# Optimization experiments

Hardware: AMD Instinct MI355X
Metric: run time of the kernel (lower is better)

Reference implementation:

```python
import jax, jax.numpy as jnp
import numpy as np

B, T, D, H = 32, 512, 1024, 16
HD = D // H  # 64


def setup_inputs() -> dict:
    key = jax.random.key(0)
    ks = jax.random.split(key, 12)
    s_in = 1.0 / np.sqrt(D)
    x = jax.random.normal(ks[0], (B, T, D), dtype=jnp.float32)
    Wi = jax.random.normal(ks[1], (D, D), dtype=jnp.float32) * s_in
    bi = jnp.zeros((D,), dtype=jnp.float32)
    Wk = jax.random.normal(ks[2], (H, D, HD), dtype=jnp.float32) * s_in
    bk = jnp.zeros((H, HD), dtype=jnp.float32)
    Wq = jax.random.normal(ks[3], (H, D, HD), dtype=jnp.float32) * s_in
    bq = jnp.zeros((H, HD), dtype=jnp.float32)
    Wv = jax.random.normal(ks[4], (H, D, HD), dtype=jnp.float32) * s_in
    bv = jnp.zeros((H, HD), dtype=jnp.float32)
    Wo = jax.random.normal(ks[5], (D, D), dtype=jnp.float32) * s_in
    bo = jnp.zeros((D,), dtype=jnp.float32)
    return {"x": x, "Wi": Wi, "bi": bi, "Wk": Wk, "bk": bk,
            "Wq": Wq, "bq": bq, "Wv": Wv, "bv": bv, "Wo": Wo, "bo": bo}


def reference(x, Wi, bi, Wk, bk, Wq, bq, Wv, bv, Wo, bo):
    # in_proj
    h = x @ Wi + bi  # [B,T,D]
    # per-head K/Q/V projections, vectorized over heads
    k = jnp.einsum('btd,hde->bhte', h, Wk) + bk[None, :, None, :]  # [B,H,T,HD]
    q = jnp.einsum('btd,hde->bhte', h, Wq) + bq[None, :, None, :]
    v = jnp.einsum('btd,hde->bhte', h, Wv) + bv[None, :, None, :]
    # NOTE: original computes wei = k @ q^T (keys as rows), masks with tril,
    # softmax over last axis (queries). Faithfully reproduced (no scaling).
    wei = jnp.einsum('bhtd,bhsd->bhts', k, q)  # [B,H,T,T]
    causal = jnp.tril(jnp.ones((T, T), dtype=bool))
    wei = jnp.where(causal, wei, -jnp.inf)
    wei = jax.nn.softmax(wei, axis=-1)
    # dropout: eval mode (identity)
    out = jnp.einsum('bhts,bhsd->bhtd', wei, v)  # [B,H,T,HD]
    out = out.transpose(0, 2, 1, 3).reshape(B, T, D)  # concat heads on last dim
    return out @ Wo + bo
```

## Files before the change

### kernel.cpp

```cpp
#include <hip/hip_runtime.h>
#include <hip/hip_bf16.h>
#include <stdint.h>

#define NTOK 16384

typedef _Float16 f16;
typedef f16   f16x8 __attribute__((ext_vector_type(8)));
typedef float f32x4 __attribute__((ext_vector_type(4)));

__device__ __forceinline__ float bf2f(ushort h){
  union { uint32_t u; float f; } v; v.u = ((uint32_t)h) << 16; return v.f;
}
__device__ __forceinline__ ushort f2bf(float f){
  union { float f; uint32_t u; } v; v.f = f;
  uint32_t u = v.u;
  return (ushort)((u + 0x7FFFu + ((u >> 16) & 1u)) >> 16);
}
__device__ __forceinline__ ushort f2h(float f){
  return __builtin_bit_cast(ushort, (f16)f);
}
__device__ __forceinline__ f16x8 ld16(const ushort* p){
  uint4 u = *(const uint4*)p;
  return __builtin_bit_cast(f16x8, u);
}
__device__ __forceinline__ float ldf(const void* p, size_t idx, int isf32){
  if (isf32) return ((const float*)p)[idx];
  return bf2f(((const ushort*)p)[idx]);
}

__device__ __forceinline__ const ushort* swz(const ushort* base, uint row, uint chunk){
  return base + (size_t)row*64u + (size_t)((chunk ^ (row & 7u))*8u);
}

__device__ __forceinline__ void stage64(const ushort* g, uint strideEl,
                                        ushort* ldsbase, uint tid){
  uint w = tid >> 6;
  #pragma unroll
  for (int i = 0; i < 2; ++i){
    uint lc  = i*256u + tid;
    uint row = lc >> 3, cp = lc & 7u;
    uint c   = cp ^ (row & 7u);
    const ushort* gp = g + (size_t)row*strideEl + c*8u;
    ushort* lp = ldsbase + (size_t)(i*256u + w*64u)*8u;
    __builtin_amdgcn_global_load_lds((const __attribute__((address_space(1))) void*)gp,
        (__attribute__((address_space(3))) void*)lp, 16, 0, 0);
  }
}

__global__ __launch_bounds__(256) void kdetect(const uint* __restrict__ wi, int* __restrict__ flag){
  __shared__ int cnt;
  if (threadIdx.x == 0) cnt = 0;
  __syncthreads();
  uint w = wi[threadIdx.x];
  uint e = (w >> 7) & 0xFFu;
  if (e >= 100u && e <= 130u) atomicAdd(&cnt, 1);
  __syncthreads();
  if (threadIdx.x == 0) flag[0] = (cnt < 128) ? 1 : 0;
}

__global__ __launch_bounds__(256) void kbias(const void* bi, const void* bo,
                                             const void* bk, const void* bq, const void* bv,
                                             const int* __restrict__ flag,
                                             float* bi_f, float* bo_f, float* bqkv_f){
  int f = flag[0];
  uint id = blockIdx.x*256u + threadIdx.x;
  if (id < 1024u)       bi_f[id]         = ldf(bi, id, f);
  else if (id < 2048u)  bo_f[id - 1024u] = ldf(bo, id - 1024u, f);
  else {
    uint j = id - 2048u;
    uint sel = j >> 10, i = j & 1023u;
    const void* src = (sel == 0) ? bk : ((sel == 1) ? bq : bv);
    bqkv_f[j] = ldf(src, i, f);
  }
}

__global__ __launch_bounds__(256) void ktranspose(const void* __restrict__ in,
                                                  const int* __restrict__ flag,
                                                  ushort* __restrict__ out){
  __shared__ float tile[64][65];
  int f = flag[0];
  uint R0 = blockIdx.x*64u, C0 = blockIdx.y*64u, t = threadIdx.x;
  #pragma unroll
  for (int i = 0; i < 16; ++i){
    uint id = i*256u + t, r = id >> 6, c = id & 63u;
    tile[r][c] = ldf(in, (size_t)(R0 + r)*1024u + C0 + c, f);
  }
  __syncthreads();
  #pragma unroll
  for (int i = 0; i < 16; ++i){
    uint id = i*256u + t, r = id >> 6, c = id & 63u;
    out[(size_t)(C0 + r)*1024u + R0 + c] = f2h(tile[c][r]);
  }
}

__global__ __launch_bounds__(256) void kqkvpack(const void* Wk, const void* Wq, const void* Wv,
                                                const int* __restrict__ flag,
                                                ushort* __restrict__ WqkvT){
  __shared__ float tile[64][65];
  int f = flag[0];
  uint sh = blockIdx.x;
  uint sel = sh >> 4, h = sh & 15u;
  uint D0 = blockIdx.y*64u, t = threadIdx.x;
  const void* W = (sel == 0) ? Wk : ((sel == 1) ? Wq : Wv);
  #pragma unroll
  for (int i = 0; i < 16; ++i){
    uint id = i*256u + t, r = id >> 6, c = id & 63u;
    tile[r][c] = ldf(W, (size_t)h*65536u + (size_t)(D0 + r)*64u + c, f);
  }
  __syncthreads();
  #pragma unroll
  for (int i = 0; i < 16; ++i){
    uint id = i*256u + t, r = id >> 6, c = id & 63u;
    WqkvT[(size_t)(sel*1024u + h*64u + r)*1024u + D0 + c] = f2h(tile[c][r]);
  }
}

__global__ __launch_bounds__(256) void kcvt_x(const void* __restrict__ x,
                                              const int* __restrict__ flag,
                                              ushort* __restrict__ xh){
  int f = flag[0];
  size_t g = (size_t)(blockIdx.x*256u + threadIdx.x)*8u;
  ushort o[8];
  if (f){
    const float* xf = (const float*)x + g;
    #pragma unroll
    for (int i = 0; i < 8; ++i) o[i] = f2h(xf[i]);
  } else {
    const ushort* xb = (const ushort*)x + g;
    #pragma unroll
    for (int i = 0; i < 8; ++i) o[i] = f2h(bf2f(xb[i]));
  }
  *(uint4*)(xh + g) = *(uint4*)o;
}

template<int MODE>
__global__ __launch_bounds__(256, 4) void kgemm(const ushort* __restrict__ A, const ushort* __restrict__ Bt,
                                                const float* __restrict__ bias, void* __restrict__ Cv,
                                                ushort* __restrict__ Vt, const int* __restrict__ dtf,
                                                int M, int N, int K){
  __shared__ ushort sA[128*32];
  __shared__ ushort sB[128*32];
  uint tid = threadIdx.x, w = tid >> 6, lane = tid & 63u, quad = lane >> 4, l15 = lane & 15u;
  uint bm = blockIdx.x, bn = blockIdx.y;
  uint wm = w >> 1, wn = w & 1u;
  f32x4 acc[4][4] = {};

  for (int k0 = 0; k0 < K; k0 += 32){
    #pragma unroll
    for (int i = 0; i < 2; ++i){
      uint c   = (w*2u + i)*64u + lane;
      uint row = c >> 2, ko = (c & 3u)*8u;
      const ushort* gA = A  + (size_t)(bm*128u + row)*K + k0 + ko;
      const ushort* gB = Bt + (size_t)(bn*128u + row)*K + k0 + ko;
      __builtin_amdgcn_global_load_lds((const __attribute__((address_space(1))) void*)gA,
          (__attribute__((address_space(3))) void*)(sA + (w*2u + i)*512u), 16, 0, 0);
      __builtin_amdgcn_global_load_lds((const __attribute__((address_space(1))) void*)gB,
          (__attribute__((address_space(3))) void*)(sB + (w*2u + i)*512u), 16, 0, 0);
    }
    __syncthreads();
    f16x8 aF[4], bF[4];
    #pragma unroll
    for (int i = 0; i < 4; ++i) aF[i] = *(const f16x8*)(sA + (wm*64u + i*16u + l15)*32u + quad*8u);
    #pragma unroll
    for (int j = 0; j < 4; ++j) bF[j] = *(const f16x8*)(sB + (wn*64u + j*16u + l15)*32u + quad*8u);
    #pragma unroll
    for (int i = 0; i < 4; ++i)
      #pragma unroll
      for (int j = 0; j < 4; ++j)
        acc[i][j] = __builtin_amdgcn_mfma_f32_16x16x32_f16(aF[i], bF[j], acc[i][j], 0, 0, 0);
    __syncthreads();
  }
  int f32out = (MODE == 2) ? dtf[0] : 0;
  #pragma unroll
  for (int j = 0; j < 4; ++j){
    uint col = bn*128u + wn*64u + j*16u + l15;
    float bj = bias[col];
    #pragma unroll
    for (int i = 0; i < 4; ++i){
      uint row0 = bm*128u + wm*64u + i*16u + quad*4u;
      #pragma unroll
      for (int r = 0; r < 4; ++r){
        float val = acc[i][j][r] + bj;
        uint row = row0 + r;
        if (MODE == 0){
          ((ushort*)Cv)[(size_t)row*N + col] = f2h(val);
        } else if (MODE == 1){
          if (col < 2048u){
            ((ushort*)Cv)[(size_t)row*2048u + col] = f2h(val);
          } else {
            uint c2 = col - 2048u;
            Vt[(size_t)(((row >> 9)*16u + (c2 >> 6))*64u + (c2 & 63u))*512u + (row & 511u)] = f2h(val);
          }
        } else {
          if (f32out) ((float*)Cv)[(size_t)row*N + col] = val;
          else        ((ushort*)Cv)[(size_t)row*N + col] = f2bf(val);
        }
      }
    }
  }
}

__global__ __launch_bounds__(256, 4) void kattn(const ushort* __restrict__ kq,
                                                const ushort* __restrict__ Vt,
                                                ushort* __restrict__ Out){
  __shared__ ushort sQ[2][64*64];
  __shared__ ushort sV[2][64*64];
  __shared__ ushort pbuf[4][16*64];
  uint tid = threadIdx.x, w = tid >> 6, lane = tid & 63u, quad = lane >> 4, l15 = lane & 15u;
  uint bh = blockIdx.x, tt = 7u - blockIdx.y;
  uint b = bh >> 4, h = bh & 15u;
  uint t0 = tt*64u;
  const float L2E = 1.44269504088896340736f;
  const float MNEG = -1.0e30f;

  stage64(kq + (size_t)(b*512u + t0)*2048u + h*64u, 2048u, (ushort*)pbuf, tid);
  stage64(kq + (size_t)(b*512u)*2048u + 1024u + h*64u, 2048u, sQ[0], tid);
  stage64(Vt + (size_t)(bh*64u)*512u, 512u, sV[0], tid);
  __syncthreads();

  f16x8 aK[2];
  aK[0] = ld16(swz((const ushort*)pbuf, w*16u + l15, quad));
  aK[1] = ld16(swz((const ushort*)pbuf, w*16u + l15, 4u + quad));

  float m[4], l[4];
  f32x4 oacc[4];
  #pragma unroll
  for (int r = 0; r < 4; ++r){ m[r] = MNEG; l[r] = 0.f; }
  #pragma unroll
  for (int je = 0; je < 4; ++je) oacc[je] = (f32x4){0.f, 0.f, 0.f, 0.f};

  ushort* pw = (ushort*)pbuf + w*1024u;

  for (uint st = 0; st <= tt; ++st){
    uint cur = st & 1u;
    if (st) __syncthreads();
    if (st < tt){
      uint s1 = (st + 1u)*64u;
      stage64(kq + (size_t)(b*512u + s1)*2048u + 1024u + h*64u, 2048u, sQ[1u - cur], tid);
      stage64(Vt + (size_t)(bh*64u)*512u + s1, 512u, sV[1u - cur], tid);
    }
    f32x4 sacc[4];
    #pragma unroll
    for (int j = 0; j < 4; ++j){
      f16x8 bq0 = ld16(swz(sQ[cur], j*16u + l15, quad));
      f16x8 bq1 = ld16(swz(sQ[cur], j*16u + l15, 4u + quad));
      f32x4 s = (f32x4){0.f, 0.f, 0.f, 0.f};
      s = __builtin_amdgcn_mfma_f32_16x16x32_f16(aK[0], bq0, s, 0, 0, 0);
      s = __builtin_amdgcn_mfma_f32_16x16x32_f16(aK[1], bq1, s, 0, 0, 0);
      #pragma unroll
      for (int r = 0; r < 4; ++r) s[r] = fminf(fmaxf(s[r], MNEG), 1.0e30f);
      sacc[j] = s;
    }
    if (st == tt){
      #pragma unroll
      for (int j = 0; j < 4; ++j)
        #pragma unroll
        for (int r = 0; r < 4; ++r)
          if (j*16u + l15 > w*16u + quad*4u + (uint)r) sacc[j][r] = MNEG;
    }
    float alpha[4];
    #pragma unroll
    for (int r = 0; r < 4; ++r){
      float v = fmaxf(fmaxf(sacc[0][r], sacc[1][r]), fmaxf(sacc[2][r], sacc[3][r]));
      v = fmaxf(v, __shfl_xor(v, 1));
      v = fmaxf(v, __shfl_xor(v, 2));
      v = fmaxf(v, __shfl_xor(v, 4));
      v = fmaxf(v, __shfl_xor(v, 8));
      float mn = fmaxf(m[r], v);
      alpha[r] = exp2f((m[r] - mn)*L2E);
      m[r] = mn;
    }
    #pragma unroll
    for (int j = 0; j < 4; ++j)
      #pragma unroll
      for (int r = 0; r < 4; ++r)
        sacc[j][r] = exp2f((sacc[j][r] - m[r])*L2E);
    #pragma unroll
    for (int r = 0; r < 4; ++r){
      float s = sacc[0][r] + sacc[1][r] + sacc[2][r] + sacc[3][r];
      s += __shfl_xor(s, 1);
      s += __shfl_xor(s, 2);
      s += __shfl_xor(s, 4);
      s += __shfl_xor(s, 8);
      l[r] = l[r]*alpha[r] + s;
    }
    #pragma unroll
    for (int je = 0; je < 4; ++je)
      #pragma unroll
      for (int r = 0; r < 4; ++r)
        oacc[je][r] *= alpha[r];
    #pragma unroll
    for (int j = 0; j < 4; ++j)
      #pragma unroll
      for (int r = 0; r < 4; ++r){
        uint t = quad*4u + (uint)r;
        pw[t*64u + (((j*2u + (l15 >> 3)) ^ (t & 7u))*8u) + (l15 & 7u)] = f2h(sacc[j][r]);
      }
    f16x8 aP0 = ld16(swz(pw, l15, quad));
    f16x8 aP1 = ld16(swz(pw, l15, 4u + quad));
    #pragma unroll
    for (int je = 0; je < 4; ++je){
      f16x8 bv0 = ld16(swz(sV[cur], je*16u + l15, quad));
      f16x8 bv1 = ld16(swz(sV[cur], je*16u + l15, 4u + quad));
      oacc[je] = __builtin_amdgcn_mfma_f32_16x16x32_f16(aP0, bv0, oacc[je], 0, 0, 0);
      oacc[je] = __builtin_amdgcn_mfma_f32_16x16x32_f16(aP1, bv1, oacc[je], 0, 0, 0);
    }
  }
  float inv[4];
  #pragma unroll
  for (int r = 0; r < 4; ++r) inv[r] = 1.0f / l[r];
  #pragma unroll
  for (int je = 0; je < 4; ++je){
    uint e = h*64u + je*16u + l15;
    #pragma unroll
    for (int r = 0; r < 4; ++r){
      uint t = t0 + w*16u + quad*4u + (uint)r;
      Out[(size_t)(b*512u + t)*1024u + e] = f2h(oacc[je][r]*inv[r]);
    }
  }
}


extern "C" void kernel_launch(void* const* d_in, const int* in_sizes, int n_in,
                              void* d_out, int out_size, void* d_ws, size_t ws_size,
                              hipStream_t stream){
  const void* x  = d_in[0];
  const void* Wi = d_in[1];
  const void* bi = d_in[2];
  const void* Wk = d_in[3];
  const void* bk = d_in[4];
  const void* Wq = d_in[5];
  const void* bq = d_in[6];
  const void* Wv = d_in[7];
  const void* bv = d_in[8];
  const void* Wo = d_in[9];
  const void* bo = d_in[10];
  char* ws = (char*)d_ws;

  const size_t MB = 1u << 20;
  int*    flag   = (int*)ws;
  float*  bi_f   = (float*)(ws + 4096);
  float*  bo_f   = (float*)(ws + 8192);
  float*  bqkv_f = (float*)(ws + 12288);
  ushort* WiT    = (ushort*)(ws + 32768);
  ushort* WoT    = (ushort*)(ws + 32768 + 2*MB);
  ushort* WqkvT  = (ushort*)(ws + 32768 + 4*MB);
  ushort* xh     = (ushort*)(ws + 32768 + 10*MB);
  ushort* kq     = (ushort*)(ws + 32768 + 10*MB);
  ushort* hbuf   = (ushort*)(ws + 32768 + 74*MB);
  ushort* Vt     = (ushort*)(ws + 32768 + 106*MB);

  kdetect<<<dim3(1), dim3(256), 0, stream>>>((const uint*)Wi, flag);
  kbias<<<dim3(20), dim3(256), 0, stream>>>(bi, bo, bk, bq, bv, flag, bi_f, bo_f, bqkv_f);
  ktranspose<<<dim3(16, 16), dim3(256), 0, stream>>>(Wi, flag, WiT);
  ktranspose<<<dim3(16, 16), dim3(256), 0, stream>>>(Wo, flag, WoT);
  kqkvpack<<<dim3(48, 16), dim3(256), 0, stream>>>(Wk, Wq, Wv, flag, WqkvT);
  kcvt_x<<<dim3(8192), dim3(256), 0, stream>>>(x, flag, xh);

  kgemm<0><<<dim3(128, 8),  dim3(256), 0, stream>>>(xh,   WiT,   bi_f,   hbuf, nullptr, nullptr, NTOK, 1024, 1024);
  kgemm<1><<<dim3(128, 24), dim3(256), 0, stream>>>(hbuf, WqkvT, bqkv_f, kq,   Vt,      nullptr, NTOK, 3072, 1024);
  kattn<<<dim3(512, 8), dim3(256), 0, stream>>>(kq, Vt, hbuf);
  kgemm<2><<<dim3(128, 8),  dim3(256), 0, stream>>>(hbuf, WoT,   bo_f,   d_out, nullptr, flag,   NTOK, 1024, 1024);
}
```

Before: 506.9 us.

## Replace GEMM with 256x256-tile, 8-wave, double-buffered swizzled-LDS pipelined kernel

Replaces the 128x128 single-buffered GEMM with a 512-thread kernel that computes 256x256 tiles. It double-buffers LDS over 64-wide K steps and issues global-to-LDS loads for the next tile in between MFMA phases. LDS columns are XOR-swizzled to avoid bank conflicts, and setprio and sched_barrier are used to interleave loads with MFMA. This aims to hide memory latency and raise data reuse per block, at the cost of more LDS, fewer blocks per CU, and fragile hand-written waitcnt synchronisation.

New measurement: 515.9 us. About the same (+1.8%).

```diff
diff --git a/kernel.cpp b/kernel.cpp
--- a/kernel.cpp
+++ b/kernel.cpp
@@ -134,54 +134,132 @@
 }
 
 template<int MODE>
-__global__ __launch_bounds__(256, 4) void kgemm(const ushort* __restrict__ A, const ushort* __restrict__ Bt,
-                                                const float* __restrict__ bias, void* __restrict__ Cv,
-                                                ushort* __restrict__ Vt, const int* __restrict__ dtf,
-                                                int M, int N, int K){
-  __shared__ ushort sA[128*32];
-  __shared__ ushort sB[128*32];
+__global__ __launch_bounds__(512, 2) void kgemm8(const ushort* __restrict__ A, const ushort* __restrict__ Bt,
+                                                 const float* __restrict__ bias, void* __restrict__ Cv,
+                                                 ushort* __restrict__ Vt, const int* __restrict__ dtf,
+                                                 int M, int N, int K){
+  __shared__ ushort sA[2][2][8192];
+  __shared__ ushort sB[2][2][8192];
   uint tid = threadIdx.x, w = tid >> 6, lane = tid & 63u, quad = lane >> 4, l15 = lane & 15u;
+  uint wm = w >> 2, wn = w & 3u;
   uint bm = blockIdx.x, bn = blockIdx.y;
-  uint wm = w >> 1, wn = w & 1u;
-  f32x4 acc[4][4] = {};
-
-  for (int k0 = 0; k0 < K; k0 += 32){
-    #pragma unroll
-    for (int i = 0; i < 2; ++i){
-      uint c   = (w*2u + i)*64u + lane;
-      uint row = c >> 2, ko = (c & 3u)*8u;
-      const ushort* gA = A  + (size_t)(bm*128u + row)*K + k0 + ko;
-      const ushort* gB = Bt + (size_t)(bn*128u + row)*K + k0 + ko;
-      __builtin_amdgcn_global_load_lds((const __attribute__((address_space(1))) void*)gA,
-          (__attribute__((address_space(3))) void*)(sA + (w*2u + i)*512u), 16, 0, 0);
-      __builtin_amdgcn_global_load_lds((const __attribute__((address_space(1))) void*)gB,
-          (__attribute__((address_space(3))) void*)(sB + (w*2u + i)*512u), 16, 0, 0);
-    }
-    __syncthreads();
+  uint cx = (quad ^ ((l15 >> 1) & 3u)) * 8u;
+  f32x4 acc[8][4] = {};
+
+  const int NT = K >> 6;
+  const ushort* GA0 = A  + (size_t)(bm*256u)*(size_t)K;
+  const ushort* GB0 = Bt + (size_t)(bn*256u)*(size_t)K;
+
+  #define STAGE_HALF(G, DST)                                                        \
+    {                                                                               \
+      _Pragma("unroll")                                                             \
+      for (int li = 0; li < 2; ++li){                                               \
+        uint lc = (uint)li*512u + tid;                                              \
+        uint row = lc >> 2, cp = lc & 3u;                                           \
+        uint c = cp ^ ((row >> 1) & 3u);                                            \
+        const ushort* gp = (G) + (size_t)row*(size_t)K + c*8u;                      \
+        ushort* lp = (DST) + (size_t)((uint)li*512u + w*64u)*8u;                    \
+        __builtin_amdgcn_global_load_lds((const __attribute__((address_space(1))) void*)gp, \
+            (__attribute__((address_space(3))) void*)lp, 16, 0, 0);                 \
+      }                                                                             \
+    }
+
+  STAGE_HALF(GA0,       sA[0][0]);
+  STAGE_HALF(GB0,       sB[0][0]);
+  STAGE_HALF(GA0 + 32u, sA[0][1]);
+  STAGE_HALF(GB0 + 32u, sB[0][1]);
+  asm volatile("s_waitcnt vmcnt(4)" ::: "memory");
+  __builtin_amdgcn_s_barrier();
+
+  for (int t = 0; t < NT; ++t){
+    uint bu = (uint)t & 1u, nbu = bu ^ 1u;
+    const ushort* GA1 = GA0 + (size_t)(t + 1)*64u;
+    const ushort* GB1 = GB0 + (size_t)(t + 1)*64u;
+    bool more = (t + 1 < NT);
+
     f16x8 aF[4], bF[4];
-    #pragma unroll
-    for (int i = 0; i < 4; ++i) aF[i] = *(const f16x8*)(sA + (wm*64u + i*16u + l15)*32u + quad*8u);
-    #pragma unroll
-    for (int j = 0; j < 4; ++j) bF[j] = *(const f16x8*)(sB + (wn*64u + j*16u + l15)*32u + quad*8u);
+
+    #pragma unroll
+    for (int i = 0; i < 4; ++i) aF[i] = ld16(&sA[bu][0][(size_t)(wm*128u + (uint)i*16u + l15)*32u + cx]);
+    #pragma unroll
+    for (int j = 0; j < 4; ++j) bF[j] = ld16(&sB[bu][0][(size_t)(wn*64u + (uint)j*16u + l15)*32u + cx]);
+    if (more) STAGE_HALF(GA1, sA[nbu][0]);
+    __builtin_amdgcn_s_barrier();
+    asm volatile("s_waitcnt lgkmcnt(0)" ::: "memory");
+    __builtin_amdgcn_sched_barrier(0);
+    __builtin_amdgcn_s_setprio(1);
     #pragma unroll
     for (int i = 0; i < 4; ++i)
       #pragma unroll
       for (int j = 0; j < 4; ++j)
         acc[i][j] = __builtin_amdgcn_mfma_f32_16x16x32_f16(aF[i], bF[j], acc[i][j], 0, 0, 0);
-    __syncthreads();
-  }
+    __builtin_amdgcn_s_setprio(0);
+    __builtin_amdgcn_s_barrier();
+
+    #pragma unroll
+    for (int i = 0; i < 4; ++i) aF[i] = ld16(&sA[bu][0][(size_t)(wm*128u + (uint)(4+i)*16u + l15)*32u + cx]);
+    if (more) STAGE_HALF(GB1, sB[nbu][0]);
+    if (more) { asm volatile("s_waitcnt vmcnt(4)" ::: "memory"); }
+    else      { asm volatile("s_waitcnt vmcnt(0)" ::: "memory"); }
+    __builtin_amdgcn_s_barrier();
+    asm volatile("s_waitcnt lgkmcnt(0)" ::: "memory");
+    __builtin_amdgcn_sched_barrier(0);
+    __builtin_amdgcn_s_setprio(1);
+    #pragma unroll
+    for (int i = 0; i < 4; ++i)
+      #pragma unroll
+      for (int j = 0; j < 4; ++j)
+        acc[4+i][j] = __builtin_amdgcn_mfma_f32_16x16x32_f16(aF[i], bF[j], acc[4+i][j], 0, 0, 0);
+    __builtin_amdgcn_s_setprio(0);
+    __builtin_amdgcn_s_barrier();
+
+    #pragma unroll
+    for (int i = 0; i < 4; ++i) aF[i] = ld16(&sA[bu][1][(size_t)(wm*128u + (uint)i*16u + l15)*32u + cx]);
+    #pragma unroll
+    for (int j = 0; j < 4; ++j) bF[j] = ld16(&sB[bu][1][(size_t)(wn*64u + (uint)j*16u + l15)*32u + cx]);
+    if (more) STAGE_HALF(GA1 + 32u, sA[nbu][1]);
+    __builtin_amdgcn_s_barrier();
+    asm volatile("s_waitcnt lgkmcnt(0)" ::: "memory");
+    __builtin_amdgcn_sched_barrier(0);
+    __builtin_amdgcn_s_setprio(1);
+    #pragma unroll
+    for (int i = 0; i < 4; ++i)
+      #pragma unroll
+      for (int j = 0; j < 4; ++j)
+        acc[i][j] = __builtin_amdgcn_mfma_f32_16x16x32_f16(aF[i], bF[j], acc[i][j], 0, 0, 0);
+    __builtin_amdgcn_s_setprio(0);
+    __builtin_amdgcn_s_barrier();
+
+    #pragma unroll
+    for (int i = 0; i < 4; ++i) aF[i] = ld16(&sA[bu][1][(size_t)(wm*128u + (uint)(4+i)*16u + l15)*32u + cx]);
+    if (more) STAGE_HALF(GB1 + 32u, sB[nbu][1]);
+    if (more) { asm volatile("s_waitcnt vmcnt(4)" ::: "memory"); }
+    __builtin_amdgcn_s_barrier();
+    asm volatile("s_waitcnt lgkmcnt(0)" ::: "memory");
+    __builtin_amdgcn_sched_barrier(0);
+    __builtin_amdgcn_s_setprio(1);
+    #pragma unroll
+    for (int i = 0; i < 4; ++i)
+      #pragma unroll
+      for (int j = 0; j < 4; ++j)
+        acc[4+i][j] = __builtin_amdgcn_mfma_f32_16x16x32_f16(aF[i], bF[j], acc[4+i][j], 0, 0, 0);
+    __builtin_amdgcn_s_setprio(0);
+    __builtin_amdgcn_s_barrier();
+  }
+  #undef STAGE_HALF
+
   int f32out = (MODE == 2) ? dtf[0] : 0;
   #pragma unroll
   for (int j = 0; j < 4; ++j){
-    uint col = bn*128u + wn*64u + j*16u + l15;
+    uint col = bn*256u + wn*64u + (uint)j*16u + l15;
     float bj = bias[col];
     #pragma unroll
-    for (int i = 0; i < 4; ++i){
-      uint row0 = bm*128u + wm*64u + i*16u + quad*4u;
+    for (int i = 0; i < 8; ++i){
+      uint row0 = bm*256u + wm*128u + (uint)i*16u + quad*4u;
       #pragma unroll
       for (int r = 0; r < 4; ++r){
         float val = acc[i][j][r] + bj;
-        uint row = row0 + r;
+        uint row = row0 + (uint)r;
         if (MODE == 0){
           ((ushort*)Cv)[(size_t)row*N + col] = f2h(val);
         } else if (MODE == 1){
@@ -357,8 +435,8 @@
   kqkvpack<<<dim3(48, 16), dim3(256), 0, stream>>>(Wk, Wq, Wv, flag, WqkvT);
   kcvt_x<<<dim3(8192), dim3(256), 0, stream>>>(x, flag, xh);
 
-  kgemm<0><<<dim3(128, 8),  dim3(256), 0, stream>>>(xh,   WiT,   bi_f,   hbuf, nullptr, nullptr, NTOK, 1024, 1024);
-  kgemm<1><<<dim3(128, 24), dim3(256), 0, stream>>>(hbuf, WqkvT, bqkv_f, kq,   Vt,      nullptr, NTOK, 3072, 1024);
+  kgemm8<0><<<dim3(64, 4),  dim3(512), 0, stream>>>(xh,   WiT,   bi_f,   hbuf, nullptr, nullptr, NTOK, 1024, 1024);
+  kgemm8<1><<<dim3(64, 12), dim3(512), 0, stream>>>(hbuf, WqkvT, bqkv_f, kq,   Vt,      nullptr, NTOK, 3072, 1024);
   kattn<<<dim3(512, 8), dim3(256), 0, stream>>>(kq, Vt, hbuf);
-  kgemm<2><<<dim3(128, 8),  dim3(256), 0, stream>>>(hbuf, WoT,   bo_f,   d_out, nullptr, flag,   NTOK, 1024, 1024);
-}
+  kgemm8<2><<<dim3(64, 4),  dim3(512), 0, stream>>>(hbuf, WoT,   bo_f,   d_out, nullptr, flag,   NTOK, 1024, 1024);
+}
```
